# Kernel tuning notes

Measured on AMD Instinct MI355X. Metric: run time of the kernel, lower is better.

Reference implementation:

```python
import jax, jax.numpy as jnp
import numpy as np

N_NODES = 100000
N_EDGES = 6400000
F_IN = 128
F_OUT = 16


def setup_inputs() -> dict:
    key = jax.random.key(0)
    k1, k2, k3 = jax.random.split(key, 3)
    x = jax.random.normal(k1, (N_NODES, F_IN), dtype=jnp.float32)
    edge_index = jax.random.randint(k2, (2, N_EDGES), 0, N_NODES, dtype=jnp.int64)
    W = jax.random.normal(k3, (F_IN, F_OUT), dtype=jnp.float32) / np.sqrt(F_IN)
    b = jnp.zeros((F_OUT,), dtype=jnp.float32)
    return {"x": x, "edge_index": edge_index, "W": W, "b": b}


def reference(x, edge_index, W, b):
    # GCNConv (PyG defaults: add self-loops, symmetric normalization) -> tanh -> mean pool
    N = x.shape[0]
    loops = jnp.arange(N, dtype=edge_index.dtype)
    row = jnp.concatenate([edge_index[0], loops])  # source nodes
    col = jnp.concatenate([edge_index[1], loops])  # target nodes
    # degree of target nodes (edge weight 1.0)
    deg = jax.ops.segment_sum(jnp.ones(row.shape[0], dtype=x.dtype), col, num_segments=N)
    dinv = jnp.where(deg > 0, jax.lax.rsqrt(deg), 0.0)
    norm = dinv[row] * dinv[col]  # [E+N]
    h = x @ W  # [N, F_OUT] transform first (cheaper than transforming messages)
    msgs = h[row] * norm[:, None]  # gather + scale
    out = jax.ops.segment_sum(msgs, col, num_segments=N) + b  # scatter-add
    h = jnp.tanh(out)
    # MeanAggregation over all nodes -> single graph embedding [1, F_OUT]
    return jnp.mean(h, axis=0, keepdims=True)
```

## Files before the change

kernel.cpp:

```cpp
#include <hip/hip_runtime.h>
#include <math.h>

#define N_NODES 100000
#define N_EDGES 6400000
#define F_IN 128
#define F_OUT 16
#define NB 391
#define NBLK 1600
#define EPB 4000
#define LOCW 392
#define KPB 4
#define ACCN (NB * 256 * F_OUT)
#define QSCALE 1024.0f
#define QINV   (1.0f / 1024.0f)
#define FIN_GRID 640

__global__ void __launch_bounds__(256) count_kernel(const int* __restrict__ col,
                                                    int* __restrict__ loc,
                                                    int* __restrict__ deg) {
    __shared__ int hist[NB];
    const int t = threadIdx.x, k = blockIdx.x;
    const int z0 = k * 63;
    for (int j = t; j < 63; j += 256)
        if (z0 + j < N_NODES) deg[z0 + j] = 0;
    for (int i = t; i < NB; i += 256) hist[i] = 0;
    __syncthreads();
    const int e0 = k * EPB;
    for (int i = t; i < EPB; i += 256) atomicAdd(&hist[col[e0 + i] >> 8], 1);
    __syncthreads();
    for (int b = t; b < NB; b += 256) loc[k * LOCW + b] = hist[b];
}

__global__ void __launch_bounds__(256) desta_kernel(const int* __restrict__ loc,
        int* __restrict__ destT, int* __restrict__ total) {
    __shared__ int tsum[256];
    const int t = threadIdx.x, b = blockIdx.x;
    int v[7]; int s = 0;
    #pragma unroll
    for (int j = 0; j < 7; j++) {
        int k = t * 7 + j;
        v[j] = (k < NBLK) ? loc[k * LOCW + b] : 0;
        s += v[j];
    }
    tsum[t] = s;
    __syncthreads();
    for (int off = 1; off < 256; off <<= 1) {
        int a = (t >= off) ? tsum[t - off] : 0;
        __syncthreads();
        tsum[t] += a;
        __syncthreads();
    }
    int run = tsum[t] - s;
    #pragma unroll
    for (int j = 0; j < 7; j++) {
        int k = t * 7 + j;
        if (k < NBLK) destT[(size_t)b * NBLK + k] = run;
        run += v[j];
    }
    if (t == 255) total[b] = tsum[255];
}

__global__ void destb_kernel(const int* __restrict__ total, int* __restrict__ boffs) {
    __shared__ int lds[512];
    const int t = threadIdx.x;
    int v = (t < NB) ? total[t] : 0;
    lds[t] = v; __syncthreads();
    for (int off = 1; off < 512; off <<= 1) {
        int a = (t >= off) ? lds[t - off] : 0; __syncthreads();
        lds[t] += a; __syncthreads();
    }
    if (t < NB) boffs[t] = lds[t] - v;
    if (t == NB) boffs[NB] = N_EDGES;
}

__global__ void __launch_bounds__(256) place_kernel(const int* __restrict__ row,
        const int* __restrict__ col, const int* __restrict__ destT,
        const int* __restrict__ boffs, unsigned int* __restrict__ packed) {
    __shared__ int hist[NB];
    __shared__ int scanb[512];
    __shared__ int base[NB];
    __shared__ int gadj[NB];
    __shared__ unsigned int tile[EPB];
    __shared__ unsigned short tileb[EPB];
    const int t = threadIdx.x, k = blockIdx.x;
    const int e0 = k * EPB;
    int myc[16], myr[16];
    #pragma unroll
    for (int j = 0; j < 16; j++) {
        int idx = t + j * 256;
        if (idx < EPB) { myc[j] = col[e0 + idx]; myr[j] = row[e0 + idx]; }
        else { myc[j] = -1; myr[j] = 0; }
    }
    for (int i = t; i < NB; i += 256) hist[i] = 0;
    __syncthreads();
    #pragma unroll
    for (int j = 0; j < 16; j++)
        if (myc[j] >= 0) atomicAdd(&hist[myc[j] >> 8], 1);
    __syncthreads();
    scanb[t] = (t < NB) ? hist[t] : 0;
    scanb[t + 256] = (t + 256 < NB) ? hist[t + 256] : 0;
    __syncthreads();
    for (int off = 1; off < 512; off <<= 1) {
        int a  = (t >= off) ? scanb[t - off] : 0;
        int a2 = scanb[t + 256 - off];
        __syncthreads();
        scanb[t] += a; scanb[t + 256] += a2;
        __syncthreads();
    }
    if (t < NB) base[t] = scanb[t] - hist[t];
    if (t + 256 < NB) base[t + 256] = scanb[t + 256] - hist[t + 256];
    __syncthreads();
    for (int bb = t; bb < NB; bb += 256) {
        gadj[bb] = boffs[bb] + destT[(size_t)bb * NBLK + k] - base[bb];
        hist[bb] = 0;
    }
    __syncthreads();
    #pragma unroll
    for (int j = 0; j < 16; j++) {
        if (myc[j] >= 0) {
            int bb = myc[j] >> 8;
            int pos = base[bb] + atomicAdd(&hist[bb], 1);
            tile[pos] = ((unsigned)myr[j] << 8) | (unsigned)(myc[j] & 255);
            tileb[pos] = (unsigned short)bb;
        }
    }
    __syncthreads();
    for (int i = t; i < EPB; i += 256)
        packed[gadj[tileb[i]] + i] = tile[i];
}

__global__ void __launch_bounds__(256) deg_kernel(const unsigned int* __restrict__ packed,
        const int* __restrict__ boffs, int* __restrict__ deg) {
    __shared__ int dh[256];
    const int t = threadIdx.x;
    dh[t] = 0;
    __syncthreads();
    const int b = blockIdx.x, part = blockIdx.y;
    const int s = boffs[b], e = boffs[b + 1];
    const int chunk = (e - s + 3) >> 2;
    const int cs = s + part * chunk;
    const int ce = min(cs + chunk, e);
    for (int i = cs + t; i < ce; i += 256)
        atomicAdd(&dh[packed[i] & 255u], 1);
    __syncthreads();
    const int node = (b << 8) + t;
    if (node < N_NODES && dh[t]) atomicAdd(&deg[node], dh[t]);
}

__global__ void __launch_bounds__(256) gemm_kernel(const float* __restrict__ x,
        const float* __restrict__ W, const int* __restrict__ deg,
        short* __restrict__ gq) {
    __shared__ float Ws[F_IN * F_OUT];
    __shared__ float xs[16 * 132];
    const int tid = threadIdx.x;
    const int n0 = blockIdx.x * 16;
    const float4* W4 = (const float4*)W;
    for (int i = tid; i < 512; i += 256) ((float4*)Ws)[i] = W4[i];
    const float4* x4 = (const float4*)(x + (size_t)n0 * F_IN);
    for (int i = tid; i < 512; i += 256) {
        int n = i >> 5, j = i & 31;
        *(float4*)(xs + n * 132 + j * 4) = x4[i];
    }
    __syncthreads();
    const int node = tid >> 4, f = tid & 15;
    const float* xr = &xs[node * 132];
    float acc = 0.f;
    #pragma unroll 8
    for (int k = 0; k < F_IN; k++) acc += xr[k] * Ws[k * 16 + f];
    const float dinvn = rsqrtf((float)deg[n0 + node] + 1.0f);
    float v = acc * dinvn * QSCALE;
    v = fminf(fmaxf(v, -32000.f), 32000.f);
    gq[n0 * 16 + tid] = (short)__float2int_rn(v);
}

__global__ void __launch_bounds__(256) scatter_kernel(
        const unsigned int* __restrict__ packed, const int* __restrict__ boffs,
        const short* __restrict__ gq, int* __restrict__ accp) {
    __shared__ int sacc[256 * F_OUT];
    const int t = threadIdx.x;
    for (int i = t; i < 256 * F_OUT; i += 256) sacc[i] = 0;
    __syncthreads();
    const int b = blockIdx.x, part = blockIdx.y;
    const int s = boffs[b], e = boffs[b + 1];
    const int chunk = (e - s + KPB - 1) / KPB;
    const int cs = s + part * chunk;
    const int ce = min(cs + chunk, e);
    const int f = t & 15, eg = t >> 4;
    int i = cs + eg;
    for (; i + 48 < ce; i += 64) {
        unsigned p0 = packed[i];
        unsigned p1 = packed[i + 16];
        unsigned p2 = packed[i + 32];
        unsigned p3 = packed[i + 48];
        int v0 = gq[(p0 >> 8) * 16 + f];
        int v1 = gq[(p1 >> 8) * 16 + f];
        int v2 = gq[(p2 >> 8) * 16 + f];
        int v3 = gq[(p3 >> 8) * 16 + f];
        atomicAdd(&sacc[((p0 & 255u) << 4) + f], v0);
        atomicAdd(&sacc[((p1 & 255u) << 4) + f], v1);
        atomicAdd(&sacc[((p2 & 255u) << 4) + f], v2);
        atomicAdd(&sacc[((p3 & 255u) << 4) + f], v3);
    }
    for (; i < ce; i += 16) {
        unsigned p0 = packed[i];
        atomicAdd(&sacc[((p0 & 255u) << 4) + f], (int)gq[(p0 >> 8) * 16 + f]);
    }
    __syncthreads();
    const int nbase = b << 8;
    int* dst = accp + (size_t)part * ACCN + ((size_t)nbase << 4);
    for (int j = t; j < 256 * F_OUT; j += 256)
        if (nbase + (j >> 4) < N_NODES) dst[j] = sacc[j];
}

__global__ void __launch_bounds__(256) finalize_kernel(const int* __restrict__ accp,
        const short* __restrict__ gq, const int* __restrict__ deg,
        const float* __restrict__ b, double* __restrict__ dsum,
        int* __restrict__ done, float* __restrict__ out) {
    __shared__ float s[4][16];
    __shared__ int lastflag;
    const int tid = threadIdx.x;
    const int f = tid & 15;
    const float bf = b[f];
    float local = 0.f;
    for (int i = blockIdx.x * blockDim.x + tid; i < N_NODES * F_OUT;
         i += gridDim.x * blockDim.x) {
        const int n = i >> 4;
        int ai = accp[i] + accp[ACCN + i] + accp[2 * ACCN + i] + accp[3 * ACCN + i]
               + (int)gq[i];
        float dinvn = rsqrtf((float)deg[n] + 1.0f);
        local += tanhf(dinvn * ((float)ai * QINV) + bf);
    }
    local += __shfl_down(local, 32);
    local += __shfl_down(local, 16);
    const int lane = tid & 63, wave = tid >> 6;
    if (lane < 16) s[wave][lane] = local;
    __syncthreads();
    if (tid < 16) {
        float v = s[0][tid] + s[1][tid] + s[2][tid] + s[3][tid];
        atomicAdd(&dsum[tid], (double)v);
    }
    if (tid == 0) {
        __threadfence();
        lastflag = (atomicAdd(done, 1) == (int)gridDim.x - 1);
    }
    __syncthreads();
    if (lastflag && tid < 16) {
        double v = atomicAdd(&dsum[tid], 0.0);
        out[tid] = (float)(v * (1.0 / (double)N_NODES));
    }
}

extern "C" void kernel_launch(void* const* d_in, const int* in_sizes, int n_in,
                              void* d_out, int out_size, void* d_ws, size_t ws_size,
                              hipStream_t stream) {
    const float* x  = (const float*)d_in[0];
    const int*   ei = (const int*)d_in[1];
    const float* W  = (const float*)d_in[2];
    const float* b  = (const float*)d_in[3];
    float* out = (float*)d_out;

    const int* row = ei;
    const int* col = ei + N_EDGES;

    char* p = (char*)d_ws;
    double*       dsum   = (double*)p;        p += 16 * 8;
    int*          done   = (int*)p;           p += 16;
    int*          total  = (int*)p;           p += 1568;
    int*          boffs  = (int*)p;           p += (NB + 1) * 4;
    int*          deg    = (int*)p;           p += (size_t)N_NODES * 4;
    short*        gq     = (short*)p;         p += (size_t)N_NODES * F_OUT * 2;
    unsigned int* packed = (unsigned int*)p;  p += (size_t)N_EDGES * 4;
    char*         shared = p;
    int*          loc    = (int*)shared;
    int*          destT  = (int*)(shared + (size_t)NBLK * LOCW * 4);
    int*          accp   = (int*)shared;

    hipMemsetAsync(dsum, 0, 16 * 8 + 16, stream);

    count_kernel   <<<NBLK, 256, 0, stream>>>(col, loc, deg);
    desta_kernel   <<<NB, 256, 0, stream>>>(loc, destT, total);
    destb_kernel   <<<1, 512, 0, stream>>>(total, boffs);
    place_kernel   <<<NBLK, 256, 0, stream>>>(row, col, destT, boffs, packed);
    deg_kernel     <<<dim3(NB, 4), 256, 0, stream>>>(packed, boffs, deg);
    gemm_kernel    <<<N_NODES / 16, 256, 0, stream>>>(x, W, deg, gq);
    scatter_kernel <<<dim3(NB, KPB), 256, 0, stream>>>(packed, boffs, gq, accp);
    finalize_kernel<<<FIN_GRID, 256, 0, stream>>>(accp, gq, deg, b, dsum, done, out);
}
```

Measured before the change: 265.7 us.

## Merge scatter partials with global atomics and double scatter splits per bucket

The scatter kernel no longer writes four separate partial accumulator copies that finalize has to sum. Each block now atomically adds its nonzero shared-memory sums into one global accumulator, which count_kernel zeroes. This lets the split factor per bucket rise from four to eight, and the inner gather loop is unrolled to eight edges per iteration for more memory-level parallelism. The cost is global atomic traffic and the extra work of zeroing the accumulator, in exchange for less partial-array write and read bandwidth.

```diff
diff --git a/kernel.cpp b/kernel.cpp
--- a/kernel.cpp
+++ b/kernel.cpp
@@ -9,20 +9,22 @@
 #define NBLK 1600
 #define EPB 4000
 #define LOCW 392
-#define KPB 4
-#define ACCN (NB * 256 * F_OUT)
+#define KPB 8
 #define QSCALE 1024.0f
 #define QINV   (1.0f / 1024.0f)
 #define FIN_GRID 640
 
 __global__ void __launch_bounds__(256) count_kernel(const int* __restrict__ col,
                                                     int* __restrict__ loc,
-                                                    int* __restrict__ deg) {
+                                                    int* __restrict__ deg,
+                                                    int* __restrict__ acc) {
     __shared__ int hist[NB];
     const int t = threadIdx.x, k = blockIdx.x;
     const int z0 = k * 63;
     for (int j = t; j < 63; j += 256)
         if (z0 + j < N_NODES) deg[z0 + j] = 0;
+    const int a0 = k * 1000;
+    for (int j = t; j < 1000; j += 256) acc[a0 + j] = 0;
     for (int i = t; i < NB; i += 256) hist[i] = 0;
     __syncthreads();
     const int e0 = k * EPB;
@@ -175,7 +177,7 @@
 
 __global__ void __launch_bounds__(256) scatter_kernel(
         const unsigned int* __restrict__ packed, const int* __restrict__ boffs,
-        const short* __restrict__ gq, int* __restrict__ accp) {
+        const short* __restrict__ gq, int* __restrict__ acc) {
     __shared__ int sacc[256 * F_OUT];
     const int t = threadIdx.x;
     for (int i = t; i < 256 * F_OUT; i += 256) sacc[i] = 0;
@@ -187,19 +189,31 @@
     const int ce = min(cs + chunk, e);
     const int f = t & 15, eg = t >> 4;
     int i = cs + eg;
-    for (; i + 48 < ce; i += 64) {
+    for (; i + 112 < ce; i += 128) {
         unsigned p0 = packed[i];
         unsigned p1 = packed[i + 16];
         unsigned p2 = packed[i + 32];
         unsigned p3 = packed[i + 48];
+        unsigned p4 = packed[i + 64];
+        unsigned p5 = packed[i + 80];
+        unsigned p6 = packed[i + 96];
+        unsigned p7 = packed[i + 112];
         int v0 = gq[(p0 >> 8) * 16 + f];
         int v1 = gq[(p1 >> 8) * 16 + f];
         int v2 = gq[(p2 >> 8) * 16 + f];
         int v3 = gq[(p3 >> 8) * 16 + f];
+        int v4 = gq[(p4 >> 8) * 16 + f];
+        int v5 = gq[(p5 >> 8) * 16 + f];
+        int v6 = gq[(p6 >> 8) * 16 + f];
+        int v7 = gq[(p7 >> 8) * 16 + f];
         atomicAdd(&sacc[((p0 & 255u) << 4) + f], v0);
         atomicAdd(&sacc[((p1 & 255u) << 4) + f], v1);
         atomicAdd(&sacc[((p2 & 255u) << 4) + f], v2);
         atomicAdd(&sacc[((p3 & 255u) << 4) + f], v3);
+        atomicAdd(&sacc[((p4 & 255u) << 4) + f], v4);
+        atomicAdd(&sacc[((p5 & 255u) << 4) + f], v5);
+        atomicAdd(&sacc[((p6 & 255u) << 4) + f], v6);
+        atomicAdd(&sacc[((p7 & 255u) << 4) + f], v7);
     }
     for (; i < ce; i += 16) {
         unsigned p0 = packed[i];
@@ -207,12 +221,14 @@
     }
     __syncthreads();
     const int nbase = b << 8;
-    int* dst = accp + (size_t)part * ACCN + ((size_t)nbase << 4);
-    for (int j = t; j < 256 * F_OUT; j += 256)
-        if (nbase + (j >> 4) < N_NODES) dst[j] = sacc[j];
-}
-
-__global__ void __launch_bounds__(256) finalize_kernel(const int* __restrict__ accp,
+    for (int j = t; j < 256 * F_OUT; j += 256) {
+        int v = sacc[j];
+        if (v && nbase + (j >> 4) < N_NODES)
+            atomicAdd(&acc[((size_t)nbase << 4) + j], v);
+    }
+}
+
+__global__ void __launch_bounds__(256) finalize_kernel(const int* __restrict__ acc,
         const short* __restrict__ gq, const int* __restrict__ deg,
         const float* __restrict__ b, double* __restrict__ dsum,
         int* __restrict__ done, float* __restrict__ out) {
@@ -225,8 +241,7 @@
     for (int i = blockIdx.x * blockDim.x + tid; i < N_NODES * F_OUT;
          i += gridDim.x * blockDim.x) {
         const int n = i >> 4;
-        int ai = accp[i] + accp[ACCN + i] + accp[2 * ACCN + i] + accp[3 * ACCN + i]
-               + (int)gq[i];
+        int ai = acc[i] + (int)gq[i];
         float dinvn = rsqrtf((float)deg[n] + 1.0f);
         local += tanhf(dinvn * ((float)ai * QINV) + bf);
     }
@@ -270,19 +285,18 @@
     int*          deg    = (int*)p;           p += (size_t)N_NODES * 4;
     short*        gq     = (short*)p;         p += (size_t)N_NODES * F_OUT * 2;
     unsigned int* packed = (unsigned int*)p;  p += (size_t)N_EDGES * 4;
-    char*         shared = p;
-    int*          loc    = (int*)shared;
-    int*          destT  = (int*)(shared + (size_t)NBLK * LOCW * 4);
-    int*          accp   = (int*)shared;
+    int*          acc    = (int*)p;           p += (size_t)N_NODES * F_OUT * 4;
+    int*          loc    = (int*)p;           p += (size_t)NBLK * LOCW * 4;
+    int*          destT  = (int*)p;
 
     hipMemsetAsync(dsum, 0, 16 * 8 + 16, stream);
 
-    count_kernel   <<<NBLK, 256, 0, stream>>>(col, loc, deg);
+    count_kernel   <<<NBLK, 256, 0, stream>>>(col, loc, deg, acc);
     desta_kernel   <<<NB, 256, 0, stream>>>(loc, destT, total);
     destb_kernel   <<<1, 512, 0, stream>>>(total, boffs);
     place_kernel   <<<NBLK, 256, 0, stream>>>(row, col, destT, boffs, packed);
     deg_kernel     <<<dim3(NB, 4), 256, 0, stream>>>(packed, boffs, deg);
     gemm_kernel    <<<N_NODES / 16, 256, 0, stream>>>(x, W, deg, gq);
-    scatter_kernel <<<dim3(NB, KPB), 256, 0, stream>>>(packed, boffs, gq, accp);
-    finalize_kernel<<<FIN_GRID, 256, 0, stream>>>(accp, gq, deg, b, dsum, done, out);
-}
+    scatter_kernel <<<dim3(NB, KPB), 256, 0, stream>>>(packed, boffs, gq, acc);
+    finalize_kernel<<<FIN_GRID, 256, 0, stream>>>(acc, gq, deg, b, dsum, done, out);
+}
```

Result: no change. 267.7 us (+0.8%).
